# Optimization experiments

Hardware: AMD Instinct MI355X
Metric: run time of the kernel (lower is better)

Reference implementation:

```python
import jax, jax.numpy as jnp
import numpy as np
from jax import lax

KH = KW = 3
STRIDE = 1
PAD = 1
DIL = 1
DG = 1  # deformable groups


def setup_inputs() -> dict:
    key = jax.random.key(0)
    k1, k2, k3 = jax.random.split(key, 3)
    B, Cin, H, W = 4, 64, 128, 128
    Cout = 64
    x = jax.random.normal(k1, (B, Cin, H, W), jnp.float32)
    # main conv weight ~ uniform(-1/sqrt(Cin*kh*kw), ...) scale
    weight = jax.random.normal(k2, (Cout, Cin, KH, KW), jnp.float32) * 0.04
    bias = jnp.zeros((Cout,), jnp.float32)
    # offset/mask conv: small weights so offsets stay near the regular grid
    offset_w = jax.random.normal(k3, (DG * 3 * KH * KW, Cin, KH, KW), jnp.float32) * 0.01
    offset_b = jnp.zeros((DG * 3 * KH * KW,), jnp.float32)
    return dict(x=x, weight=weight, bias=bias, offset_w=offset_w, offset_b=offset_b)


def _conv2d(x, w, b):
    out = lax.conv_general_dilated(
        x, w, window_strides=(STRIDE, STRIDE), padding=[(PAD, PAD), (PAD, PAD)],
        rhs_dilation=(DIL, DIL), dimension_numbers=('NCHW', 'OIHW', 'NCHW'))
    return out + b[None, :, None, None]


def _dcn_forward(x, weight, bias, offset_w, offset_b):
    B, Cin, H, W = x.shape
    Cout = weight.shape[0]
    K = KH * KW
    # offset / mask branch (ordinary conv)
    om = _conv2d(x, offset_w, offset_b)            # [B, 3*DG*K, Ho, Wo]
    Ho, Wo = om.shape[2], om.shape[3]
    o1, o2, m = jnp.split(om, 3, axis=1)           # chunk into dy, dx, mask
    dy = o1.reshape(B, DG, K, Ho, Wo)
    dx = o2.reshape(B, DG, K, Ho, Wo)
    mask = jax.nn.sigmoid(m).reshape(B, DG, K, Ho, Wo)
    # regular grid sample positions per kernel tap
    ki = jnp.arange(KH)
    kj = jnp.arange(KW)
    base_h = (jnp.arange(Ho) * STRIDE - PAD)[None, :] + (ki * DIL)[:, None]   # [KH, Ho]
    base_w = (jnp.arange(Wo) * STRIDE - PAD)[None, :] + (kj * DIL)[:, None]   # [KW, Wo]
    base_h = jnp.broadcast_to(base_h[:, None, :, None], (KH, KW, Ho, Wo)).reshape(K, Ho, Wo)
    base_w = jnp.broadcast_to(base_w[None, :, None, :], (KH, KW, Ho, Wo)).reshape(K, Ho, Wo)
    h = base_h[None, None].astype(dy.dtype) + dy   # [B, DG, K, Ho, Wo] float
    w = base_w[None, None].astype(dx.dtype) + dx
    h0 = jnp.floor(h)
    w0 = jnp.floor(w)
    lh = h - h0
    lw = w - w0
    h0i = h0.astype(jnp.int32)
    w0i = w0.astype(jnp.int32)
    Cg = Cin // DG
    xg = x.reshape(B, DG, Cg, H * W)

    def gather(hi, wi):
        # zero-padded bilinear corner gather, shared across the group's channels
        valid = (hi >= 0) & (hi < H) & (wi >= 0) & (wi < W)
        idx = jnp.clip(hi, 0, H - 1) * W + jnp.clip(wi, 0, W - 1)        # [B,DG,K,Ho,Wo]
        idxf = jnp.broadcast_to(idx.reshape(B, DG, 1, K * Ho * Wo), (B, DG, Cg, K * Ho * Wo))
        v = jnp.take_along_axis(xg, idxf, axis=3).reshape(B, DG, Cg, K, Ho, Wo)
        return v * valid[:, :, None].astype(v.dtype)

    wgt = lambda a, b_: (a * b_)[:, :, None]       # -> [B,DG,1,K,Ho,Wo]
    val = (wgt(1 - lh, 1 - lw) * gather(h0i, w0i)
           + wgt(1 - lh, lw) * gather(h0i, w0i + 1)
           + wgt(lh, 1 - lw) * gather(h0i + 1, w0i)
           + wgt(lh, lw) * gather(h0i + 1, w0i + 1))
    cols = val * mask[:, :, None]                  # modulated columns [B,DG,Cg,K,Ho,Wo]
    wk = weight.reshape(Cout, DG, Cg, K)
    out = jnp.einsum('bgckhw,ogck->bohw', cols, wk) + bias[None, :, None, None]
    return out


def reference(x, weight, bias, offset_w, offset_b):
    return _dcn_forward(x, weight, bias, offset_w, offset_b)
```

## Files before the change

### kernel.cpp

```cpp
#include <hip/hip_runtime.h>
#include <hip/hip_fp16.h>

#define B_   4
#define CIN  64
#define HH   128
#define WW   128
#define COUT 64
#define HW   (HH * WW)
#define KK   9

typedef float    f32x4 __attribute__((ext_vector_type(4)));
typedef _Float16 f16x8 __attribute__((ext_vector_type(8)));

union U4 {
    uint4     q;
    uint32_t  u[4];
    __half2   h2[4];
    f16x8     v;
};

#define MFMA16(a, b, c) __builtin_amdgcn_mfma_f32_16x16x32_f16((a).v, (b).v, (c), 0, 0, 0)

__global__ __launch_bounds__(256)
void prep_kernel(const float* __restrict__ w,
                 const float* __restrict__ ow,
                 __half* __restrict__ wpack,
                 __half* __restrict__ wop) {
    int i = blockIdx.x * 256 + threadIdx.x;
    if (i < 36864) {
        int j = i & 7, l = (i >> 3) & 63, s = i >> 9;
        int t = s >> 2;
        int rr = t * 32 + ((l >> 4) << 3) + j;
        int c = rr & 63, k = rr >> 6;
        int o = (s & 3) * 16 + (l & 15);
        wpack[i] = __float2half(w[(o * CIN + c) * KK + k]);
    } else {
        int i2 = i - 36864;
        int j = i2 & 7, l = (i2 >> 3) & 63, s = i2 >> 9;
        int t = s >> 1;
        int rr = t * 32 + ((l >> 4) << 3) + j;
        int c = rr & 63, k = rr >> 6;
        int o = (s & 1) * 16 + (l & 15);
        wop[i2] = __float2half((o < 27) ? ow[(o * CIN + c) * KK + k] : 0.f);
    }
}

__global__ __launch_bounds__(512, 2)
void dcn_fused_kernel(const float* __restrict__ x,
                      const __half* __restrict__ wop,
                      const float* __restrict__ ob,
                      const __half* __restrict__ wpack,
                      const float* __restrict__ bias,
                      float* __restrict__ out) {
    int bid0 = blockIdx.x;
    int bid  = (bid0 & 7) * 32 + (bid0 >> 3);
    int b = bid >> 6, rp = bid & 63;
    int ho0 = rp * 2;
    int tid = threadIdx.x;
    int w = tid >> 6, l = tid & 63;
    int p = l & 15, grp = l >> 4, grp16 = grp << 4;
    int r = w >> 2, q = w & 3;
    int ho = ho0 + r;
    int wo0 = q * 32;

    __shared__ __align__(16) char  xs[131072];
    __shared__ __half lomh[8][27][34];

    const float* xbF = x + (size_t)b * CIN * HW;

#pragma unroll
    for (int it = 0; it < 16; ++it) {
        int cg  = it & 7;
        int pix = (it >> 3) * 512 + tid;
        int rr = pix >> 7, col = pix & 127;
        int srow = min(max(ho0 - 3 + rr, 0), HH - 1);
        const float* xp = xbF + (size_t)(cg * 8) * HW + srow * WW + col;
        uint32_t u[4];
#pragma unroll
        for (int j = 0; j < 4; ++j) {
            __half2 h = __floats2half2_rn(xp[(size_t)(2 * j) * HW],
                                          xp[(size_t)(2 * j + 1) * HW]);
            u[j] = *(uint32_t*)&h;
        }
        *(uint4*)(xs + (((rr << 14) + (col << 7) + (cg << 4)) ^ ((col & 7) << 4)))
            = *(const uint4*)u;
    }
    __syncthreads();

    {
        const uint4* wpo = (const uint4*)wop + l;
        int aad[2][9], asw[2][9];
        uint32_t avm[2][9];
#pragma unroll
        for (int m = 0; m < 2; ++m)
#pragma unroll
        for (int k = 0; k < 9; ++k) {
            int ki = k / 3, kj = k % 3;
            int hh = ho + ki - 1;
            int cr = wo0 + m * 16 + p + kj - 1;
            bool v = ((unsigned)hh < (unsigned)HH) && ((unsigned)cr < (unsigned)WW);
            int slot = r + ki + 2;
            int cc = min(max(cr, 0), WW - 1);
            aad[m][k] = (slot << 14) + (cc << 7) + grp16;
            asw[m][k] = (cc & 7) << 4;
            avm[m][k] = v ? 0xffffffffu : 0u;
        }
        f32x4 oacc[2][2] = {};
#pragma unroll
        for (int t = 0; t < 18; ++t) {
            int k = t >> 1, half = t & 1;
            U4 a0, a1;
            a0.q = *(const uint4*)(xs + ((aad[0][k] + (half << 6)) ^ asw[0][k]));
            a1.q = *(const uint4*)(xs + ((aad[1][k] + (half << 6)) ^ asw[1][k]));
#pragma unroll
            for (int i = 0; i < 4; ++i) { a0.u[i] &= avm[0][k]; a1.u[i] &= avm[1][k]; }
            U4 b0, b1;
            b0.q = wpo[(t * 2 + 0) * 64];
            b1.q = wpo[(t * 2 + 1) * 64];
            oacc[0][0] = MFMA16(a0, b0, oacc[0][0]);
            oacc[0][1] = MFMA16(a0, b1, oacc[0][1]);
            oacc[1][0] = MFMA16(a1, b0, oacc[1][0]);
            oacc[1][1] = MFMA16(a1, b1, oacc[1][1]);
        }
#pragma unroll
        for (int m = 0; m < 2; ++m)
#pragma unroll
        for (int nt = 0; nt < 2; ++nt) {
            int oc = nt * 16 + (l & 15);
            if (oc < 27) {
                float bv = ob[oc];
#pragma unroll
                for (int i = 0; i < 4; ++i) {
                    float vv = oacc[m][nt][i] + bv;
                    if (oc >= 18) vv = 1.f / (1.f + __expf(-vv));
                    lomh[w][oc][m * 16 + grp * 4 + i] = __float2half(vv);
                }
            }
        }
    }

    f32x4 acc[2][4] = {};
    const uint4* wpm = (const uint4*)wpack + l;

#pragma unroll
    for (int k = 0; k < 9; ++k) {
        int ch0[2], ch1[2], cw0[2], cw1[2];
        __half2 hwA[2], hwB[2], hwC[2], hwD[2];
        int okall = 1;
#pragma unroll
        for (int m = 0; m < 2; ++m) {
            int px = m * 16 + p;
            float dy = __half2float(lomh[w][k][px]);
            float dx = __half2float(lomh[w][9 + k][px]);
            float mk = __half2float(lomh[w][18 + k][px]);
            float hf = (float)(ho - 1 + k / 3) + dy;
            float wf = (float)(wo0 + px - 1 + k % 3) + dx;
            float h0f = floorf(hf), w0f = floorf(wf);
            float lh = hf - h0f, lw = wf - w0f;
            int h0 = (int)h0f, w0i = (int)w0f;
            int h1 = h0 + 1, w1i = w0i + 1;
            bool vh0 = (unsigned)h0 < (unsigned)HH, vh1 = (unsigned)h1 < (unsigned)HH;
            bool vw0 = (unsigned)w0i < (unsigned)WW, vw1 = (unsigned)w1i < (unsigned)WW;
            int c0 = min(max(h0, 0), HH - 1), c1 = min(max(h1, 0), HH - 1);
            int d0 = min(max(w0i, 0), WW - 1), d1 = min(max(w1i, 0), WW - 1);
            ch0[m] = c0; ch1[m] = c1; cw0[m] = d0; cw1[m] = d1;
            float fA = (vh0 && vw0) ? (1.f - lh) * (1.f - lw) * mk : 0.f;
            float fB = (vh0 && vw1) ? (1.f - lh) * lw * mk : 0.f;
            float fC = (vh1 && vw0) ? lh * (1.f - lw) * mk : 0.f;
            float fD = (vh1 && vw1) ? lh * lw * mk : 0.f;
            hwA[m] = __float2half2_rn(fA); hwB[m] = __float2half2_rn(fB);
            hwC[m] = __float2half2_rn(fC); hwD[m] = __float2half2_rn(fD);
            int s0 = c0 + 3 - ho0, s1 = c1 + 3 - ho0;
            okall &= (int)((unsigned)s0 <= 7u) & (int)((unsigned)s1 <= 7u);
        }
        int okw = __all(okall);

#pragma unroll
        for (int half = 0; half < 2; ++half) {
            int t = 2 * k + half;
            int hb = (half << 6) + grp16;
            U4 bf0, bf1, bf2, bf3;
            bf0.q = wpm[(t * 4 + 0) * 64];
            bf1.q = wpm[(t * 4 + 1) * 64];
            bf2.q = wpm[(t * 4 + 2) * 64];
            bf3.q = wpm[(t * 4 + 3) * 64];
            U4 a[2];
            if (okw) {
#pragma unroll
                for (int m = 0; m < 2; ++m) {
                    int s0 = ch0[m] + 3 - ho0, s1 = ch1[m] + 3 - ho0;
                    U4 u0, u1, u2, u3;
                    u0.q = *(const uint4*)(xs + (((s0 << 14) + (cw0[m] << 7) + hb) ^ ((cw0[m] & 7) << 4)));
                    u1.q = *(const uint4*)(xs + (((s0 << 14) + (cw1[m] << 7) + hb) ^ ((cw1[m] & 7) << 4)));
                    u2.q = *(const uint4*)(xs + (((s1 << 14) + (cw0[m] << 7) + hb) ^ ((cw0[m] & 7) << 4)));
                    u3.q = *(const uint4*)(xs + (((s1 << 14) + (cw1[m] << 7) + hb) ^ ((cw1[m] & 7) << 4)));
#pragma unroll
                    for (int i = 0; i < 4; ++i)
                        a[m].h2[i] = __hfma2(hwD[m], u3.h2[i],
                                     __hfma2(hwC[m], u2.h2[i],
                                     __hfma2(hwB[m], u1.h2[i],
                                     __hmul2(hwA[m], u0.h2[i]))));
                }
            } else {
                const float* cbase = xbF + (size_t)(32 * half + grp * 8) * HW;
#pragma unroll
                for (int m = 0; m < 2; ++m) {
                    U4 u0, u1, u2, u3;
#pragma unroll
                    for (int j = 0; j < 4; ++j) {
                        const float* p0 = cbase + (size_t)(2 * j) * HW;
                        const float* p1 = cbase + (size_t)(2 * j + 1) * HW;
                        int i00 = ch0[m] * WW + cw0[m], i01 = ch0[m] * WW + cw1[m];
                        int i10 = ch1[m] * WW + cw0[m], i11 = ch1[m] * WW + cw1[m];
                        __half2 h;
                        h = __floats2half2_rn(p0[i00], p1[i00]); u0.u[j] = *(uint32_t*)&h;
                        h = __floats2half2_rn(p0[i01], p1[i01]); u1.u[j] = *(uint32_t*)&h;
                        h = __floats2half2_rn(p0[i10], p1[i10]); u2.u[j] = *(uint32_t*)&h;
                        h = __floats2half2_rn(p0[i11], p1[i11]); u3.u[j] = *(uint32_t*)&h;
                    }
#pragma unroll
                    for (int i = 0; i < 4; ++i)
                        a[m].h2[i] = __hfma2(hwD[m], u3.h2[i],
                                     __hfma2(hwC[m], u2.h2[i],
                                     __hfma2(hwB[m], u1.h2[i],
                                     __hmul2(hwA[m], u0.h2[i]))));
                }
            }
            acc[0][0] = MFMA16(a[0], bf0, acc[0][0]);
            acc[0][1] = MFMA16(a[0], bf1, acc[0][1]);
            acc[0][2] = MFMA16(a[0], bf2, acc[0][2]);
            acc[0][3] = MFMA16(a[0], bf3, acc[0][3]);
            acc[1][0] = MFMA16(a[1], bf0, acc[1][0]);
            acc[1][1] = MFMA16(a[1], bf1, acc[1][1]);
            acc[1][2] = MFMA16(a[1], bf2, acc[1][2]);
            acc[1][3] = MFMA16(a[1], bf3, acc[1][3]);
        }
    }

#pragma unroll
    for (int m = 0; m < 2; ++m)
#pragma unroll
    for (int nt = 0; nt < 4; ++nt) {
        int oc = nt * 16 + (l & 15);
        float bv = bias[oc];
        f32x4 s;
#pragma unroll
        for (int i = 0; i < 4; ++i) s[i] = acc[m][nt][i] + bv;
        *(f32x4*)(out + ((size_t)(b * COUT + oc)) * HW + ho * WW + wo0 + m * 16 + grp * 4) = s;
    }
}

extern "C" void kernel_launch(void* const* d_in, const int* in_sizes, int n_in,
                              void* d_out, int out_size, void* d_ws, size_t ws_size,
                              hipStream_t stream) {
    const float* x    = (const float*)d_in[0];
    const float* wgt  = (const float*)d_in[1];
    const float* bias = (const float*)d_in[2];
    const float* ow   = (const float*)d_in[3];
    const float* ob   = (const float*)d_in[4];
    float* out = (float*)d_out;

    char* ws = (char*)d_ws;
    __half* wpack = (__half*)ws;
    __half* wop   = (__half*)(ws + 73728);

    prep_kernel<<<216, 256, 0, stream>>>(wgt, ow, wpack, wop);
    dcn_fused_kernel<<<B_ * HH / 2, 512, 0, stream>>>(x, wop, ob, wpack, bias, out);
}
```

Before: 96.32 us.

## Split row-pair tiles into half-width blocks with smaller halo smem window

Each block now handles two output rows by 64 columns with 256 threads, instead of two full rows with 512 threads. The shared-memory input window shrinks from 8 rows by 128 columns to 6 rows by 72 columns. The grid doubles to 512 blocks and the smaller LDS footprint allows more blocks per CU, which should improve occupancy and load balance. The offset/mask buffer is also re-laid out so each pixel's dy/dx/mask for a tap can be read in one 8-byte load. In exchange, each block reloads extra halo columns, and samples falling outside the narrower window take the slow global-memory path more often.

Result: no change. 97.38 us (+1.1%).

```diff
diff --git a/kernel.cpp b/kernel.cpp
--- a/kernel.cpp
+++ b/kernel.cpp
@@ -8,6 +8,10 @@
 #define COUT 64
 #define HW   (HH * WW)
 #define KK   9
+
+#define WROWS 6
+#define WCOLS 72
+#define ROWSTRIDE (WCOLS * 128)
 
 typedef float    f32x4 __attribute__((ext_vector_type(4)));
 typedef _Float16 f16x8 __attribute__((ext_vector_type(8)));
@@ -45,7 +49,7 @@
     }
 }
 
-__global__ __launch_bounds__(512, 2)
+__global__ __launch_bounds__(256, 2)
 void dcn_fused_kernel(const float* __restrict__ x,
                       const __half* __restrict__ wop,
                       const float* __restrict__ ob,
@@ -53,37 +57,42 @@
                       const float* __restrict__ bias,
                       float* __restrict__ out) {
     int bid0 = blockIdx.x;
-    int bid  = (bid0 & 7) * 32 + (bid0 >> 3);
-    int b = bid >> 6, rp = bid & 63;
+    int bid  = (bid0 & 7) * 64 + (bid0 >> 3);
+    int ch = bid & 1, rp = (bid >> 1) & 63, b = bid >> 7;
     int ho0 = rp * 2;
+    int wstart = ch * 64 - 4;
     int tid = threadIdx.x;
     int w = tid >> 6, l = tid & 63;
     int p = l & 15, grp = l >> 4, grp16 = grp << 4;
-    int r = w >> 2, q = w & 3;
+    int r = w >> 1, q = w & 1;
     int ho = ho0 + r;
-    int wo0 = q * 32;
-
-    __shared__ __align__(16) char  xs[131072];
-    __shared__ __half lomh[8][27][34];
+    int wo0 = ch * 64 + q * 32;
+
+    __shared__ __align__(16) char xs[WROWS * ROWSTRIDE];
+    __shared__ __half lompH[4][32][9][4];
 
     const float* xbF = x + (size_t)b * CIN * HW;
 
 #pragma unroll
-    for (int it = 0; it < 16; ++it) {
-        int cg  = it & 7;
-        int pix = (it >> 3) * 512 + tid;
-        int rr = pix >> 7, col = pix & 127;
-        int srow = min(max(ho0 - 3 + rr, 0), HH - 1);
-        const float* xp = xbF + (size_t)(cg * 8) * HW + srow * WW + col;
-        uint32_t u[4];
-#pragma unroll
-        for (int j = 0; j < 4; ++j) {
-            __half2 h = __floats2half2_rn(xp[(size_t)(2 * j) * HW],
-                                          xp[(size_t)(2 * j + 1) * HW]);
-            u[j] = *(uint32_t*)&h;
-        }
-        *(uint4*)(xs + (((rr << 14) + (col << 7) + (cg << 4)) ^ ((col & 7) << 4)))
-            = *(const uint4*)u;
+    for (int it = 0; it < 14; ++it) {
+        int idx = it * 256 + tid;
+        if (idx < WROWS * WCOLS * 8) {
+            int wc = idx % WCOLS;
+            int tmp = idx / WCOLS;
+            int cg = tmp & 7, rr = tmp >> 3;
+            int srow = min(max(ho0 - 2 + rr, 0), HH - 1);
+            int scol = min(max(wstart + wc, 0), WW - 1);
+            const float* xp = xbF + (size_t)(cg * 8) * HW + srow * WW + scol;
+            uint32_t u[4];
+#pragma unroll
+            for (int j = 0; j < 4; ++j) {
+                __half2 h = __floats2half2_rn(xp[(size_t)(2 * j) * HW],
+                                              xp[(size_t)(2 * j + 1) * HW]);
+                u[j] = *(uint32_t*)&h;
+            }
+            *(uint4*)(xs + ((rr * ROWSTRIDE + (wc << 7) + (cg << 4)) ^ ((wc & 7) << 4)))
+                = *(const uint4*)u;
+        }
     }
     __syncthreads();
 
@@ -99,10 +108,11 @@
             int hh = ho + ki - 1;
             int cr = wo0 + m * 16 + p + kj - 1;
             bool v = ((unsigned)hh < (unsigned)HH) && ((unsigned)cr < (unsigned)WW);
-            int slot = r + ki + 2;
+            int slot = r + ki + 1;
             int cc = min(max(cr, 0), WW - 1);
-            aad[m][k] = (slot << 14) + (cc << 7) + grp16;
-            asw[m][k] = (cc & 7) << 4;
+            int wcx = cc - wstart;
+            aad[m][k] = slot * ROWSTRIDE + (wcx << 7) + grp16;
+            asw[m][k] = (wcx & 7) << 4;
             avm[m][k] = v ? 0xffffffffu : 0u;
         }
         f32x4 oacc[2][2] = {};
@@ -129,11 +139,12 @@
             int oc = nt * 16 + (l & 15);
             if (oc < 27) {
                 float bv = ob[oc];
+                int f = oc / 9, kk = oc - f * 9;
 #pragma unroll
                 for (int i = 0; i < 4; ++i) {
                     float vv = oacc[m][nt][i] + bv;
-                    if (oc >= 18) vv = 1.f / (1.f + __expf(-vv));
-                    lomh[w][oc][m * 16 + grp * 4 + i] = __float2half(vv);
+                    if (f == 2) vv = 1.f / (1.f + __expf(-vv));
+                    lompH[w][m * 16 + grp * 4 + i][kk][f] = __float2half(vv);
                 }
             }
         }
@@ -150,9 +161,12 @@
 #pragma unroll
         for (int m = 0; m < 2; ++m) {
             int px = m * 16 + p;
-            float dy = __half2float(lomh[w][k][px]);
-            float dx = __half2float(lomh[w][9 + k][px]);
-            float mk = __half2float(lomh[w][18 + k][px]);
+            uint2 lv = *(const uint2*)&lompH[w][px][k][0];
+            __half2 d01 = *(__half2*)&lv.x;
+            __half2 d2x = *(__half2*)&lv.y;
+            float dy = __half2float(__low2half(d01));
+            float dx = __half2float(__high2half(d01));
+            float mk = __half2float(__low2half(d2x));
             float hf = (float)(ho - 1 + k / 3) + dy;
             float wf = (float)(wo0 + px - 1 + k % 3) + dx;
             float h0f = floorf(hf), w0f = floorf(wf);
@@ -170,8 +184,10 @@
             float fD = (vh1 && vw1) ? lh * lw * mk : 0.f;
             hwA[m] = __float2half2_rn(fA); hwB[m] = __float2half2_rn(fB);
             hwC[m] = __float2half2_rn(fC); hwD[m] = __float2half2_rn(fD);
-            int s0 = c0 + 3 - ho0, s1 = c1 + 3 - ho0;
-            okall &= (int)((unsigned)s0 <= 7u) & (int)((unsigned)s1 <= 7u);
+            int s0 = c0 + 2 - ho0, s1 = c1 + 2 - ho0;
+            int e0 = d0 - wstart,  e1 = d1 - wstart;
+            okall &= (int)((unsigned)s0 <= 5u) & (int)((unsigned)s1 <= 5u)
+                   & (int)((unsigned)e0 <= 71u) & (int)((unsigned)e1 <= 71u);
         }
         int okw = __all(okall);
 
@@ -188,12 +204,13 @@
             if (okw) {
 #pragma unroll
                 for (int m = 0; m < 2; ++m) {
-                    int s0 = ch0[m] + 3 - ho0, s1 = ch1[m] + 3 - ho0;
+                    int s0 = ch0[m] + 2 - ho0, s1 = ch1[m] + 2 - ho0;
+                    int e0 = cw0[m] - wstart,  e1 = cw1[m] - wstart;
                     U4 u0, u1, u2, u3;
-                    u0.q = *(const uint4*)(xs + (((s0 << 14) + (cw0[m] << 7) + hb) ^ ((cw0[m] & 7) << 4)));
-                    u1.q = *(const uint4*)(xs + (((s0 << 14) + (cw1[m] << 7) + hb) ^ ((cw1[m] & 7) << 4)));
-                    u2.q = *(const uint4*)(xs + (((s1 << 14) + (cw0[m] << 7) + hb) ^ ((cw0[m] & 7) << 4)));
-                    u3.q = *(const uint4*)(xs + (((s1 << 14) + (cw1[m] << 7) + hb) ^ ((cw1[m] & 7) << 4)));
+                    u0.q = *(const uint4*)(xs + ((s0 * ROWSTRIDE + (e0 << 7) + hb) ^ ((e0 & 7) << 4)));
+                    u1.q = *(const uint4*)(xs + ((s0 * ROWSTRIDE + (e1 << 7) + hb) ^ ((e1 & 7) << 4)));
+                    u2.q = *(const uint4*)(xs + ((s1 * ROWSTRIDE + (e0 << 7) + hb) ^ ((e0 & 7) << 4)));
+                    u3.q = *(const uint4*)(xs + ((s1 * ROWSTRIDE + (e1 << 7) + hb) ^ ((e1 & 7) << 4)));
 #pragma unroll
                     for (int i = 0; i < 4; ++i)
                         a[m].h2[i] = __hfma2(hwD[m], u3.h2[i],
@@ -265,5 +282,5 @@
     __half* wop   = (__half*)(ws + 73728);
 
     prep_kernel<<<216, 256, 0, stream>>>(wgt, ow, wpack, wop);
-    dcn_fused_kernel<<<B_ * HH / 2, 512, 0, stream>>>(x, wop, ob, wpack, bias, out);
+    dcn_fused_kernel<<<B_ * HH, 256, 0, stream>>>(x, wop, ob, wpack, bias, out);
 }
```
